# Kernel optimization log

Measured on AMD Instinct MI355X. Metric: run time of the kernel, lower is better.

The kernel has to match this reference:

```python
import jax, jax.numpy as jnp
import numpy as np

N_NODES = 100000
N_EDGES = 320000
DIM = 256


def _graph_conv(src, dst, h, W, b):
    # DGL GraphConv, norm='both', in_feats == out_feats (aggregate-then-transform)
    ones = jnp.ones((src.shape[0],), dtype=h.dtype)
    out_deg = jnp.clip(jax.ops.segment_sum(ones, src, num_segments=N_NODES), 1.0)
    in_deg = jnp.clip(jax.ops.segment_sum(ones, dst, num_segments=N_NODES), 1.0)
    h = h * (out_deg ** -0.5)[:, None]          # src-side normalization
    agg = jax.ops.segment_sum(h[src], dst, num_segments=N_NODES)  # SpMM (copy_u, sum)
    agg = agg * (in_deg ** -0.5)[:, None]       # dst-side normalization
    return agg @ W + b


def setup_inputs() -> dict:
    key = jax.random.key(0)
    ks = jax.random.split(key, 7)
    src = jax.random.randint(ks[0], (N_EDGES,), 0, N_NODES, dtype=jnp.int32)
    dst = jax.random.randint(ks[1], (N_EDGES,), 0, N_NODES, dtype=jnp.int32)
    node_feature = jax.random.normal(ks[2], (N_NODES, DIM), dtype=jnp.float32)
    s = 1.0 / np.sqrt(DIM)
    W1 = jax.random.normal(ks[3], (DIM, DIM), dtype=jnp.float32) * s
    b1 = jnp.zeros((DIM,), dtype=jnp.float32)
    W2 = jax.random.normal(ks[4], (DIM, DIM), dtype=jnp.float32) * s
    b2 = jnp.zeros((DIM,), dtype=jnp.float32)
    return {"src": src, "dst": dst, "node_feature": node_feature,
            "W1": W1, "b1": b1, "W2": W2, "b2": b2}


def reference(src, dst, node_feature, W1, b1, W2, b2):
    h = _graph_conv(src, dst, node_feature, W1, b1)
    h = _graph_conv(src, dst, jax.nn.relu(h), W2, b2)
    return jax.nn.relu(h)
```

## Files before the change

kernel.cpp:

```cpp
#include <hip/hip_runtime.h>

#define NN 100000
#define NE 320000
#define DIM 256
#define ELLW 32
#define FEAT_BLKS (NN * DIM / 4 / 256)

typedef _Float16 half8 __attribute__((ext_vector_type(8)));
typedef _Float16 half4v __attribute__((ext_vector_type(4)));
typedef float float4v __attribute__((ext_vector_type(4)));

__global__ void k_build(const int* __restrict__ src, const int* __restrict__ dst,
                        int* __restrict__ cnt_out, int* __restrict__ cnt_in,
                        int* __restrict__ ell) {
    int e = blockIdx.x * 256 + threadIdx.x;
    if (e < NE) {
        int s = src[e], d = dst[e];
        atomicAdd(&cnt_out[s], 1);
        int slot = atomicAdd(&cnt_in[d], 1);
        if (slot < ELLW) ell[d * ELLW + slot] = s;
    }
}

__global__ __launch_bounds__(256)
void k_prep(const float* __restrict__ feat, const int* __restrict__ cnt_out,
            _Float16* __restrict__ fh,
            const float* __restrict__ W1, const float* __restrict__ W2,
            _Float16* __restrict__ WT1, _Float16* __restrict__ WT2) {
    int b = blockIdx.x;
    if (b < FEAT_BLKS) {
        int i = b * 256 + threadIdx.x;
        int row = i >> 6;
        float w = rsqrtf(fmaxf((float)cnt_out[row], 1.f));
        float4 v = reinterpret_cast<const float4*>(feat)[i];
        half4v o;
        o[0] = (_Float16)(v.x * w); o[1] = (_Float16)(v.y * w);
        o[2] = (_Float16)(v.z * w); o[3] = (_Float16)(v.w * w);
        reinterpret_cast<half4v*>(fh)[i] = o;
    } else {
        int i = (b - FEAT_BLKS) * 256 + threadIdx.x;
        int k = i >> 8, n = i & 255;
        WT1[(size_t)n * DIM + k] = (_Float16)W1[(size_t)k * DIM + n];
        WT2[(size_t)n * DIM + k] = (_Float16)W2[(size_t)k * DIM + n];
    }
}

#define LDA 264

template <typename OutT, bool PRESCALE>
__global__ __launch_bounds__(512)
void k_fused(const int* __restrict__ deg, const int* __restrict__ ell,
             const _Float16* __restrict__ T,
             const _Float16* __restrict__ WT,
             const float* __restrict__ bias,
             const int* __restrict__ cnt_in, const int* __restrict__ cnt_out,
             OutT* __restrict__ out) {
    __shared__ _Float16 As[64 * LDA];

    const int t    = threadIdx.x;
    const int lane = t & 63;
    const int w    = t >> 6;
    const int half = lane >> 5, sl = lane & 31;
    const int bm   = blockIdx.x * 64;
    const int c    = sl << 3;
    const int n0   = bm + w * 8;

    int dgv  = deg[min(n0 + (lane & 7), NN - 1)];
    int pre0 = ell[(size_t)min(n0 +     (lane >> 4), NN - 1) * ELLW + (lane & 15)];
    int pre1 = ell[(size_t)min(n0 + 4 + (lane >> 4), NN - 1) * ELLW + (lane & 15)];

    const half8 hz = {};

#define ISSUE(i, va0, vb0, va1, vb1, capv)                                     \
    {                                                                          \
        capv = 0;                                                              \
        va0 = hz; vb0 = hz; va1 = hz; vb1 = hz;                                \
        if (n0 + (i) < NN) capv = min(__shfl(dgv, (i)), ELLW);                 \
        int pr  = ((i) < 4) ? pre0 : pre1;                                     \
        int bse = ((i) & 3) * 16;                                              \
        int sa0 = __shfl(pr, bse + 0 + half);                                  \
        int sb0 = __shfl(pr, bse + 2 + half);                                  \
        int sa1 = __shfl(pr, bse + 4 + half);                                  \
        int sb1 = __shfl(pr, bse + 6 + half);                                  \
        if (0 + half < capv) va0 = *reinterpret_cast<const half8*>(T + (size_t)sa0 * DIM + c); \
        if (2 + half < capv) vb0 = *reinterpret_cast<const half8*>(T + (size_t)sb0 * DIM + c); \
        if (4 + half < capv) va1 = *reinterpret_cast<const half8*>(T + (size_t)sa1 * DIM + c); \
        if (6 + half < capv) vb1 = *reinterpret_cast<const half8*>(T + (size_t)sb1 * DIM + c); \
    }

#define CONSUME(i, va0, vb0, va1, vb1, capv)                                   \
    {                                                                          \
        float acc[8];                                                          \
        _Pragma("unroll")                                                      \
        for (int q = 0; q < 8; ++q)                                            \
            acc[q] = ((float)va0[q] + (float)vb0[q]) + ((float)va1[q] + (float)vb1[q]); \
        if (capv > 8) {             \
            int pr  = ((i) < 4) ? pre0 : pre1;                                 \
            int bse = ((i) & 3) * 16;                                          \
            _Pragma("unroll")                                                  \
            for (int e0 = 8; e0 < 16; e0 += 4) {                               \
                bool pa = e0 + half < capv, pb = e0 + 2 + half < capv;         \
                int  sa = __shfl(pr, bse + e0 + half);                         \
                int  sb = __shfl(pr, bse + e0 + 2 + half);                     \
                half8 xa = hz, xb = hz;                                        \
                if (pa) xa = *reinterpret_cast<const half8*>(T + (size_t)sa * DIM + c); \
                if (pb) xb = *reinterpret_cast<const half8*>(T + (size_t)sb * DIM + c); \
                _Pragma("unroll")                                              \
                for (int q = 0; q < 8; ++q) acc[q] += (float)xa[q] + (float)xb[q]; \
            }                                                                  \
            for (int e = 16 + half; e < capv; e += 2) {        \
                int sg = ell[(size_t)(n0 + (i)) * ELLW + e];                   \
                half8 xv = *reinterpret_cast<const half8*>(T + (size_t)sg * DIM + c); \
                _Pragma("unroll")                                              \
                for (int q = 0; q < 8; ++q) acc[q] += (float)xv[q];            \
            }                                                                  \
        }                                                                      \
        _Pragma("unroll")                                                      \
        for (int q = 0; q < 8; ++q) acc[q] += __shfl_xor(acc[q], 32);          \
        if (half == 0) {                                                       \
            half8 o;                                                           \
            _Pragma("unroll")                                                  \
            for (int q = 0; q < 8; ++q) o[q] = (_Float16)acc[q];               \
            *reinterpret_cast<half8*>(&As[(w * 8 + (i)) * LDA + c]) = o;       \
        }                                                                      \
    }

    half8 a0A, b0A, a1A, b1A, a0B, b0B, a1B, b1B;
    int capA, capB;
    ISSUE(0, a0A, b0A, a1A, b1A, capA)
    ISSUE(1, a0B, b0B, a1B, b1B, capB)
    CONSUME(0, a0A, b0A, a1A, b1A, capA)
    ISSUE(2, a0A, b0A, a1A, b1A, capA)
    CONSUME(1, a0B, b0B, a1B, b1B, capB)
    ISSUE(3, a0B, b0B, a1B, b1B, capB)
    CONSUME(2, a0A, b0A, a1A, b1A, capA)
    ISSUE(4, a0A, b0A, a1A, b1A, capA)
    CONSUME(3, a0B, b0B, a1B, b1B, capB)
    ISSUE(5, a0B, b0B, a1B, b1B, capB)
    CONSUME(4, a0A, b0A, a1A, b1A, capA)
    ISSUE(6, a0A, b0A, a1A, b1A, capA)
    CONSUME(5, a0B, b0B, a1B, b1B, capB)
    ISSUE(7, a0B, b0B, a1B, b1B, capB)
    CONSUME(6, a0A, b0A, a1A, b1A, capA)
    CONSUME(7, a0B, b0B, a1B, b1B, capB)
#undef ISSUE
#undef CONSUME

    __syncthreads();

    const int l15 = lane & 15, quad = lane >> 4;
    const int colb = w * 32;
    const _Float16* bp0 = WT + (size_t)(colb +      l15) * DIM + quad * 8;
    const _Float16* bp1 = WT + (size_t)(colb + 16 + l15) * DIM + quad * 8;

    float4v acc4[4][2] = {};
    #pragma unroll
    for (int k0 = 0; k0 < DIM; k0 += 32) {
        half8 bf0 = *reinterpret_cast<const half8*>(bp0 + k0);
        half8 bf1 = *reinterpret_cast<const half8*>(bp1 + k0);
        half8 af[4];
        #pragma unroll
        for (int mt = 0; mt < 4; ++mt)
            af[mt] = *reinterpret_cast<half8*>(&As[(mt * 16 + l15) * LDA + quad * 8 + k0]);
        #pragma unroll
        for (int mt = 0; mt < 4; ++mt) {
            acc4[mt][0] = __builtin_amdgcn_mfma_f32_16x16x32_f16(af[mt], bf0, acc4[mt][0], 0, 0, 0);
            acc4[mt][1] = __builtin_amdgcn_mfma_f32_16x16x32_f16(af[mt], bf1, acc4[mt][1], 0, 0, 0);
        }
    }

    float bc0 = bias[colb + l15];
    float bc1 = bias[colb + 16 + l15];

    #pragma unroll
    for (int mt = 0; mt < 4; ++mt) {
        #pragma unroll
        for (int r = 0; r < 4; ++r) {
            int row = bm + mt * 16 + quad * 4 + r;
            if (row < NN) {
                float s  = rsqrtf(fmaxf((float)cnt_in[row], 1.f));
                float ps = PRESCALE ? rsqrtf(fmaxf((float)cnt_out[row], 1.f)) : 1.0f;
                float v0 = fmaxf(acc4[mt][0][r] * s + bc0, 0.f) * ps;
                float v1 = fmaxf(acc4[mt][1][r] * s + bc1, 0.f) * ps;
                out[(size_t)row * DIM + colb +      l15] = (OutT)v0;
                out[(size_t)row * DIM + colb + 16 + l15] = (OutT)v1;
            }
        }
    }
}

extern "C" void kernel_launch(void* const* d_in, const int* in_sizes, int n_in,
                              void* d_out, int out_size, void* d_ws, size_t ws_size,
                              hipStream_t stream) {
    const int*   src  = (const int*)d_in[0];
    const int*   dst  = (const int*)d_in[1];
    const float* feat = (const float*)d_in[2];
    const float* W1   = (const float*)d_in[3];
    const float* b1   = (const float*)d_in[4];
    const float* W2   = (const float*)d_in[5];
    const float* b2   = (const float*)d_in[6];
    float* out = (float*)d_out;

    int*      cnt_out = (int*)d_ws;
    int*      cnt_in  = cnt_out + NN;
    int*      ell     = cnt_in + NN;
    _Float16* WT1     = (_Float16*)(ell + (size_t)NN * ELLW);
    _Float16* WT2     = WT1 + DIM * DIM;
    _Float16* fh      = WT2 + DIM * DIM;
    _Float16* h1      = fh + (size_t)NN * DIM;

    hipMemsetAsync(d_ws, 0, (size_t)2 * NN * sizeof(int), stream);

    k_build<<<(NE + 255) / 256, 256, 0, stream>>>(src, dst, cnt_out, cnt_in, ell);
    k_prep <<<FEAT_BLKS + 256, 256, 0, stream>>>(feat, cnt_out, fh, W1, W2, WT1, WT2);

    const int ggrid = (NN + 63) / 64;

    k_fused<_Float16, true ><<<ggrid, 512, 0, stream>>>(cnt_in, ell, fh, WT1, b1, cnt_in, cnt_out, h1);
    k_fused<float,    false><<<ggrid, 512, 0, stream>>>(cnt_in, ell, h1, WT2, b2, cnt_in, cnt_out, out);
}
```

Measured before the change: 365.1 us.

## Gather full rows per wave with half4 loads and deeper edge prefetch pipeline

The aggregation phase now has all 64 lanes cover one 256-wide row with half4 loads, one edge at a time, instead of splitting edges across two half-waves with half8 loads plus a cross-half shuffle reduction. The ELL table now stores source offsets premultiplied by DIM, which drops a multiply per gather. Each node's first eight edges are split into two issue stages, and four register sets are kept in flight so more independent gathers are outstanding at once. The aim is better memory-level parallelism and no cross-lane reduction. The cost is narrower loads, more registers, and more serial dependence for high-degree nodes.

```diff
diff --git a/kernel.cpp b/kernel.cpp
--- a/kernel.cpp
+++ b/kernel.cpp
@@ -18,7 +18,7 @@
         int s = src[e], d = dst[e];
         atomicAdd(&cnt_out[s], 1);
         int slot = atomicAdd(&cnt_in[d], 1);
-        if (slot < ELLW) ell[d * ELLW + slot] = s;
+        if (slot < ELLW) ell[d * ELLW + slot] = s * DIM;
     }
 }
 
@@ -60,91 +60,114 @@
     const int t    = threadIdx.x;
     const int lane = t & 63;
     const int w    = t >> 6;
-    const int half = lane >> 5, sl = lane & 31;
     const int bm   = blockIdx.x * 64;
-    const int c    = sl << 3;
     const int n0   = bm + w * 8;
-
-    int dgv  = deg[min(n0 + (lane & 7), NN - 1)];
+    const int loff = lane << 2;
+
+    int dgv  = min(deg[min(n0 + (lane & 7), NN - 1)], ELLW);
     int pre0 = ell[(size_t)min(n0 +     (lane >> 4), NN - 1) * ELLW + (lane & 15)];
     int pre1 = ell[(size_t)min(n0 + 4 + (lane >> 4), NN - 1) * ELLW + (lane & 15)];
 
-    const half8 hz = {};
-
-#define ISSUE(i, va0, vb0, va1, vb1, capv)                                     \
-    {                                                                          \
-        capv = 0;                                                              \
-        va0 = hz; vb0 = hz; va1 = hz; vb1 = hz;                                \
-        if (n0 + (i) < NN) capv = min(__shfl(dgv, (i)), ELLW);                 \
-        int pr  = ((i) < 4) ? pre0 : pre1;                                     \
-        int bse = ((i) & 3) * 16;                                              \
-        int sa0 = __shfl(pr, bse + 0 + half);                                  \
-        int sb0 = __shfl(pr, bse + 2 + half);                                  \
-        int sa1 = __shfl(pr, bse + 4 + half);                                  \
-        int sb1 = __shfl(pr, bse + 6 + half);                                  \
-        if (0 + half < capv) va0 = *reinterpret_cast<const half8*>(T + (size_t)sa0 * DIM + c); \
-        if (2 + half < capv) vb0 = *reinterpret_cast<const half8*>(T + (size_t)sb0 * DIM + c); \
-        if (4 + half < capv) va1 = *reinterpret_cast<const half8*>(T + (size_t)sa1 * DIM + c); \
-        if (6 + half < capv) vb1 = *reinterpret_cast<const half8*>(T + (size_t)sb1 * DIM + c); \
-    }
-
-#define CONSUME(i, va0, vb0, va1, vb1, capv)                                   \
-    {                                                                          \
-        float acc[8];                                                          \
-        _Pragma("unroll")                                                      \
-        for (int q = 0; q < 8; ++q)                                            \
-            acc[q] = ((float)va0[q] + (float)vb0[q]) + ((float)va1[q] + (float)vb1[q]); \
-        if (capv > 8) {             \
-            int pr  = ((i) < 4) ? pre0 : pre1;                                 \
-            int bse = ((i) & 3) * 16;                                          \
-            _Pragma("unroll")                                                  \
-            for (int e0 = 8; e0 < 16; e0 += 4) {                               \
-                bool pa = e0 + half < capv, pb = e0 + 2 + half < capv;         \
-                int  sa = __shfl(pr, bse + e0 + half);                         \
-                int  sb = __shfl(pr, bse + e0 + 2 + half);                     \
-                half8 xa = hz, xb = hz;                                        \
-                if (pa) xa = *reinterpret_cast<const half8*>(T + (size_t)sa * DIM + c); \
-                if (pb) xb = *reinterpret_cast<const half8*>(T + (size_t)sb * DIM + c); \
-                _Pragma("unroll")                                              \
-                for (int q = 0; q < 8; ++q) acc[q] += (float)xa[q] + (float)xb[q]; \
+    const half4v hz = {};
+    float a0, a1, a2, a3;
+
+#define ISSUE0(s, V0, V1, V2, V3, cap)                                         \
+    {                                                                          \
+        const int i_ = (s) >> 1;                                               \
+        cap = (n0 + i_ < NN) ? __shfl(dgv, i_) : 0;                            \
+        int pr_ = (i_ < 4) ? pre0 : pre1;                                      \
+        int b_  = (i_ & 3) << 4;                                               \
+        int s0_ = __shfl(pr_, b_ + 0), s1_ = __shfl(pr_, b_ + 1);              \
+        int s2_ = __shfl(pr_, b_ + 2), s3_ = __shfl(pr_, b_ + 3);              \
+        V0 = hz; V1 = hz; V2 = hz; V3 = hz;                                    \
+        if (cap > 0) V0 = *reinterpret_cast<const half4v*>(T + (size_t)s0_ + loff); \
+        if (cap > 1) V1 = *reinterpret_cast<const half4v*>(T + (size_t)s1_ + loff); \
+        if (cap > 2) V2 = *reinterpret_cast<const half4v*>(T + (size_t)s2_ + loff); \
+        if (cap > 3) V3 = *reinterpret_cast<const half4v*>(T + (size_t)s3_ + loff); \
+    }
+
+#define ISSUE1(s, V0, V1, V2, V3, cap)                                         \
+    {                                                                          \
+        const int i_ = (s) >> 1;                                               \
+        if (cap > 4) {                                                         \
+            int pr_ = (i_ < 4) ? pre0 : pre1;                                  \
+            int b_  = (i_ & 3) << 4;                                           \
+            int s0_ = __shfl(pr_, b_ + 4), s1_ = __shfl(pr_, b_ + 5);          \
+            int s2_ = __shfl(pr_, b_ + 6), s3_ = __shfl(pr_, b_ + 7);          \
+            V0 = hz; V1 = hz; V2 = hz; V3 = hz;                                \
+            V0 = *reinterpret_cast<const half4v*>(T + (size_t)s0_ + loff);     \
+            if (cap > 5) V1 = *reinterpret_cast<const half4v*>(T + (size_t)s1_ + loff); \
+            if (cap > 6) V2 = *reinterpret_cast<const half4v*>(T + (size_t)s2_ + loff); \
+            if (cap > 7) V3 = *reinterpret_cast<const half4v*>(T + (size_t)s3_ + loff); \
+        }                                                                      \
+    }
+
+#define CONSUME0(s, V0, V1, V2, V3)                                            \
+    {                                                                          \
+        a0 = ((float)V0[0] + (float)V1[0]) + ((float)V2[0] + (float)V3[0]);    \
+        a1 = ((float)V0[1] + (float)V1[1]) + ((float)V2[1] + (float)V3[1]);    \
+        a2 = ((float)V0[2] + (float)V1[2]) + ((float)V2[2] + (float)V3[2]);    \
+        a3 = ((float)V0[3] + (float)V1[3]) + ((float)V2[3] + (float)V3[3]);    \
+    }
+
+#define CONSUME1(s, V0, V1, V2, V3, cap)                                       \
+    {                                                                          \
+        const int i_ = (s) >> 1;                                               \
+        if (cap > 4) {                                                         \
+            a0 += ((float)V0[0] + (float)V1[0]) + ((float)V2[0] + (float)V3[0]); \
+            a1 += ((float)V0[1] + (float)V1[1]) + ((float)V2[1] + (float)V3[1]); \
+            a2 += ((float)V0[2] + (float)V1[2]) + ((float)V2[2] + (float)V3[2]); \
+            a3 += ((float)V0[3] + (float)V1[3]) + ((float)V2[3] + (float)V3[3]); \
+        }                                                                      \
+        if (cap > 8) {                                   \
+            int pr_ = (i_ < 4) ? pre0 : pre1;                                  \
+            int b_  = (i_ & 3) << 4;                                           \
+            for (int e = 8; e < cap && e < 16; ++e) {                          \
+                int se = __shfl(pr_, b_ + e);                                  \
+                half4v v = *reinterpret_cast<const half4v*>(T + (size_t)se + loff); \
+                a0 += (float)v[0]; a1 += (float)v[1];                          \
+                a2 += (float)v[2]; a3 += (float)v[3];                          \
             }                                                                  \
-            for (int e = 16 + half; e < capv; e += 2) {        \
-                int sg = ell[(size_t)(n0 + (i)) * ELLW + e];                   \
-                half8 xv = *reinterpret_cast<const half8*>(T + (size_t)sg * DIM + c); \
-                _Pragma("unroll")                                              \
-                for (int q = 0; q < 8; ++q) acc[q] += (float)xv[q];            \
+            for (int e = 16; e < cap; ++e) {      \
+                int se = ell[(size_t)(n0 + i_) * ELLW + e];                    \
+                half4v v = *reinterpret_cast<const half4v*>(T + (size_t)se + loff); \
+                a0 += (float)v[0]; a1 += (float)v[1];                          \
+                a2 += (float)v[2]; a3 += (float)v[3];                          \
             }                                                                  \
         }                                                                      \
-        _Pragma("unroll")                                                      \
-        for (int q = 0; q < 8; ++q) acc[q] += __shfl_xor(acc[q], 32);          \
-        if (half == 0) {                                                       \
-            half8 o;                                                           \
-            _Pragma("unroll")                                                  \
-            for (int q = 0; q < 8; ++q) o[q] = (_Float16)acc[q];               \
-            *reinterpret_cast<half8*>(&As[(w * 8 + (i)) * LDA + c]) = o;       \
-        }                                                                      \
-    }
-
-    half8 a0A, b0A, a1A, b1A, a0B, b0B, a1B, b1B;
-    int capA, capB;
-    ISSUE(0, a0A, b0A, a1A, b1A, capA)
-    ISSUE(1, a0B, b0B, a1B, b1B, capB)
-    CONSUME(0, a0A, b0A, a1A, b1A, capA)
-    ISSUE(2, a0A, b0A, a1A, b1A, capA)
-    CONSUME(1, a0B, b0B, a1B, b1B, capB)
-    ISSUE(3, a0B, b0B, a1B, b1B, capB)
-    CONSUME(2, a0A, b0A, a1A, b1A, capA)
-    ISSUE(4, a0A, b0A, a1A, b1A, capA)
-    CONSUME(3, a0B, b0B, a1B, b1B, capB)
-    ISSUE(5, a0B, b0B, a1B, b1B, capB)
-    CONSUME(4, a0A, b0A, a1A, b1A, capA)
-    ISSUE(6, a0A, b0A, a1A, b1A, capA)
-    CONSUME(5, a0B, b0B, a1B, b1B, capB)
-    ISSUE(7, a0B, b0B, a1B, b1B, capB)
-    CONSUME(6, a0A, b0A, a1A, b1A, capA)
-    CONSUME(7, a0B, b0B, a1B, b1B, capB)
-#undef ISSUE
-#undef CONSUME
+        half4v o;                                                              \
+        o[0] = (_Float16)a0; o[1] = (_Float16)a1;                              \
+        o[2] = (_Float16)a2; o[3] = (_Float16)a3;                              \
+        *reinterpret_cast<half4v*>(&As[(w * 8 + i_) * LDA + loff]) = o;        \
+    }
+
+    half4v A0, A1, A2, A3, B0, B1, B2, B3, C0, C1, C2, C3, D0, D1, D2, D3;
+    int cA, cB, cC, cD;
+
+    ISSUE0(0, A0, A1, A2, A3, cA)
+    ISSUE1(1, B0, B1, B2, B3, cA)
+    ISSUE0(2, C0, C1, C2, C3, cC)
+    ISSUE1(3, D0, D1, D2, D3, cC)
+    CONSUME0(0, A0, A1, A2, A3)               ISSUE0(4, A0, A1, A2, A3, cB)
+    CONSUME1(1, B0, B1, B2, B3, cA)           ISSUE1(5, B0, B1, B2, B3, cB)
+    CONSUME0(2, C0, C1, C2, C3)               ISSUE0(6, C0, C1, C2, C3, cD)
+    CONSUME1(3, D0, D1, D2, D3, cC)           ISSUE1(7, D0, D1, D2, D3, cD)
+    CONSUME0(4, A0, A1, A2, A3)               ISSUE0(8, A0, A1, A2, A3, cA)
+    CONSUME1(5, B0, B1, B2, B3, cB)           ISSUE1(9, B0, B1, B2, B3, cA)
+    CONSUME0(6, C0, C1, C2, C3)               ISSUE0(10, C0, C1, C2, C3, cC)
+    CONSUME1(7, D0, D1, D2, D3, cD)           ISSUE1(11, D0, D1, D2, D3, cC)
+    CONSUME0(8, A0, A1, A2, A3)               ISSUE0(12, A0, A1, A2, A3, cB)
+    CONSUME1(9, B0, B1, B2, B3, cA)           ISSUE1(13, B0, B1, B2, B3, cB)
+    CONSUME0(10, C0, C1, C2, C3)              ISSUE0(14, C0, C1, C2, C3, cD)
+    CONSUME1(11, D0, D1, D2, D3, cC)          ISSUE1(15, D0, D1, D2, D3, cD)
+    CONSUME0(12, A0, A1, A2, A3)
+    CONSUME1(13, B0, B1, B2, B3, cB)
+    CONSUME0(14, C0, C1, C2, C3)
+    CONSUME1(15, D0, D1, D2, D3, cD)
+#undef ISSUE0
+#undef ISSUE1
+#undef CONSUME0
+#undef CONSUME1
 
     __syncthreads();
 
```

Measured after the change: 363.9 us, median of 2. Within noise of the previous version (-0.3%).
